# Performance work log

Measured on AMD Instinct MI355X. Metric: run time of the kernel, lower is better.

The kernel has to match this reference:

```python
import jax, jax.numpy as jnp
import numpy as np

TEMP = 0.07
EPS = 1e-6
NORM_EPS = 1e-12  # F.normalize default eps
LN_EPS = 1e-5

B, D, H, W = 32, 256, 64, 64
K = 256
DFF = 2048


def _l2norm(v, axis):
    n = jnp.sqrt(jnp.sum(v * v, axis=axis, keepdims=True))
    return v / jnp.maximum(n, NORM_EPS)


def _layernorm(v, g, b):
    mu = jnp.mean(v, axis=-1, keepdims=True)
    var = jnp.mean((v - mu) ** 2, axis=-1, keepdims=True)
    return (v - mu) * jax.lax.rsqrt(var + LN_EPS) * g + b


def setup_inputs() -> dict:
    key = jax.random.key(0)
    ks = jax.random.split(key, 8)
    s1 = 1.0 / np.sqrt(D)
    s2 = 1.0 / np.sqrt(DFF)
    return {
        "x": jax.random.normal(ks[0], (B, D, H, W), jnp.float32),
        "tgt": jax.random.normal(ks[1], (B, K, D), jnp.float32),
        "w1": jax.random.uniform(ks[2], (DFF, D), jnp.float32, -s1, s1),
        "b1": jax.random.uniform(ks[3], (DFF,), jnp.float32, -s1, s1),
        "w2": jax.random.uniform(ks[4], (D, DFF), jnp.float32, -s2, s2),
        "b2": jax.random.uniform(ks[5], (D,), jnp.float32, -s2, s2),
        "g2": jnp.ones((D,), jnp.float32),
        "be2": jnp.zeros((D,), jnp.float32),
        "g3": jnp.ones((D,), jnp.float32),
        "be3": jnp.zeros((D,), jnp.float32),
    }


def reference(x, tgt, w1, b1, w2, b2, g2, be2, g3, be3):
    # slot cross-attention with L2-normalized q/k
    tn = _l2norm(tgt, axis=2)           # (b,k,d)
    xn = _l2norm(x, axis=1)             # (b,d,h,w)
    dots = jnp.einsum('bkd,bdhw->bkhw', tn, xn)
    attn = jax.nn.softmax(dots / TEMP, axis=1) + EPS          # softmax over slots
    attn = attn / jnp.sum(attn, axis=(2, 3), keepdims=True)   # spatial normalization
    tgt2 = jnp.einsum('bdhw,bkhw->bkd', x, attn)
    t = _layernorm(tgt + tgt2, g2, be2)
    # FFN (dropout = identity in eval)
    ff = jnp.maximum(t @ w1.T + b1, 0.0) @ w2.T + b2
    return _layernorm(t + ff, g3, be3)
```

## Files before the change

kernel.cpp:

```cpp
#include <hip/hip_runtime.h>
#include <hip/hip_bf16.h>

using bf16 = __hip_bfloat16;

typedef __attribute__((ext_vector_type(8))) short short8;
typedef __attribute__((ext_vector_type(4))) float f32x4;

constexpr int Bb = 32, Dd = 256, HWw = 4096, Kk = 256, Ff = 2048;
constexpr float TEMP_INV = 1.0f / 0.07f;
constexpr float EPSf = 1e-6f;
constexpr float NORM_EPSf = 1e-12f;
constexpr float LN_EPSf = 1e-5f;

static __device__ __forceinline__ float b2f(bf16 v) { return __bfloat162float(v); }
static __device__ __forceinline__ bf16 f2b(float v) { return __float2bfloat16(v); }


__global__ __launch_bounds__(64) void k_tn(const float* __restrict__ tgt,
                                           bf16* __restrict__ tnbf) {
  int row = blockIdx.x;
  int b = row >> 8, slot = row & 255;
  int lane = threadIdx.x;
  const float* src = tgt + (size_t)row * Dd + lane * 4;
  float v[4];
#pragma unroll
  for (int u = 0; u < 4; u++) v[u] = src[u];
  float ss = v[0] * v[0] + v[1] * v[1] + v[2] * v[2] + v[3] * v[3];
#pragma unroll
  for (int m = 32; m >= 1; m >>= 1) ss += __shfl_xor(ss, m, 64);
  float inv = 1.0f / fmaxf(sqrtf(ss), NORM_EPSf);
  bf16 o[4] __attribute__((aligned(8)));
#pragma unroll
  for (int u = 0; u < 4; u++) o[u] = f2b(v[u] * inv);
  int s = lane >> 3;
  int q2 = (lane >> 1) & 3;
  int jh = (lane & 1) * 4;
  size_t fi = (size_t)((slot >> 4) * 64 + q2 * 16 + (slot & 15));
  *(float2*)(tnbf + ((size_t)(b * 8 + s) * 1024 + fi) * 8 + jh) = *(float2*)o;
}

__global__ __launch_bounds__(64) void k_prew1(const float* __restrict__ w1,
                                              bf16* __restrict__ w1bf) {
  int f = blockIdx.x;
  int lane = threadIdx.x;
  const float* src = w1 + (size_t)f * Dd + lane * 4;
  bf16 o[4] __attribute__((aligned(8)));
#pragma unroll
  for (int u = 0; u < 4; u++) o[u] = f2b(src[u]);
  int s = lane >> 3;
  int q2 = (lane >> 1) & 3;
  int jh = (lane & 1) * 4;
  size_t fi = (size_t)(((f & 63) >> 4) * 64 + q2 * 16 + (f & 15));
  *(float2*)(w1bf + ((size_t)((f >> 6) * 8 + s) * 256 + fi) * 8 + jh) = *(float2*)o;
}

__global__ __launch_bounds__(64) void k_prew2(const float* __restrict__ w2,
                                              bf16* __restrict__ w2bf) {
  int d = blockIdx.x;
  int lane = threadIdx.x;
  const float* src = w2 + (size_t)d * Ff + lane * 32;
  size_t gbase = (size_t)((d >> 6) * 64 + lane) * 256;
  int fbase = ((d & 63) >> 4) * 64 + (d & 15);
#pragma unroll
  for (int q2 = 0; q2 < 4; q2++) {
    float4 v0 = *(const float4*)(src + q2 * 8);
    float4 v1 = *(const float4*)(src + q2 * 8 + 4);
    bf16 o[8] __attribute__((aligned(16)));
    o[0] = f2b(v0.x); o[1] = f2b(v0.y); o[2] = f2b(v0.z); o[3] = f2b(v0.w);
    o[4] = f2b(v1.x); o[5] = f2b(v1.y); o[6] = f2b(v1.z); o[7] = f2b(v1.w);
    *(float4*)(w2bf + (gbase + fbase + q2 * 16) * 8) = *(float4*)o;
  }
}

#define MFMA16(a, b, c) __builtin_amdgcn_mfma_f32_16x16x32_bf16(a, b, c, 0, 0, 0)

__global__ __launch_bounds__(256) void k_dots(const bf16* __restrict__ tnbf,
                                              const float* __restrict__ x,
                                              bf16* __restrict__ xb_bf,
                                              bf16* __restrict__ attn_bf,
                                              float* __restrict__ S) {
  __shared__ __align__(16) char smem[23296];
  bf16* Bs = (bf16*)smem;
  float* ssred = (float*)(smem + 16640);
  float* nxl = (float*)(smem + 20992);
  float* red = (float*)(smem + 21248);
  int b = blockIdx.x >> 6;
  int hw0 = (blockIdx.x & 63) * 64;
  int tid = threadIdx.x;
  int wave = tid >> 6, lane = tid & 63;
  int quad = lane >> 4, nl = lane & 15;

  int dp = tid >> 4;
  int ch = tid & 15;
  int qb = dp >> 2;
  int jb = (dp & 3) * 2;

  f32x4 acc[4][4];
#pragma unroll
  for (int i = 0; i < 4; i++)
#pragma unroll
    for (int j = 0; j < 4; j++) acc[i][j] = (f32x4){0.f, 0.f, 0.f, 0.f};
  float ssp[4] = {0.f, 0.f, 0.f, 0.f};

  int spx = (hw0 >> 5) + (ch >> 3);
  int q2x = (ch >> 1) & 3;
  int jx = (ch & 1) * 4;

  float4 va4[2], vb4[2];
#pragma unroll
  for (int q = 0; q < 2; q++) {
    const float* xr = x + (size_t)((b << 8) + q * 32 + 2 * dp) * HWw + hw0 + ch * 4;
    va4[q] = *(const float4*)xr;
    vb4[q] = *(const float4*)(xr + HWw);
  }
  short8 afp[4];
  {
    const bf16* ts0 = tnbf + (size_t)(b * 8) * 1024 * 8;
#pragma unroll
    for (int mt = 0; mt < 4; mt++)
      afp[mt] = *(const short8*)(ts0 + (size_t)(((wave << 2) + mt) * 64 + lane) * 8);
  }

#pragma unroll 1
  for (int p = 0; p < 4; p++) {
    bf16* bsb = Bs + (p & 1) * 2 * 2080;
    bf16 paS[2][4] __attribute__((aligned(8)));
    bf16 pbS[2][4] __attribute__((aligned(8)));
#pragma unroll
    for (int q = 0; q < 2; q++) {
      float vva[4] = {va4[q].x, va4[q].y, va4[q].z, va4[q].w};
      float vvb[4] = {vb4[q].x, vb4[q].y, vb4[q].z, vb4[q].w};
#pragma unroll
      for (int jj = 0; jj < 4; jj++) {
        ssp[jj] += vva[jj] * vva[jj] + vvb[jj] * vvb[jj];
        paS[q][jj] = f2b(vva[jj]);
        pbS[q][jj] = f2b(vvb[jj]);
      }
#pragma unroll
      for (int jj = 0; jj < 4; jj++) {
        int hwl = ch * 4 + jj;
        int nt = hwl >> 4;
        int li = (qb << 4) | (hwl & 15);
        union { bf16 h[2]; unsigned int u; } pk;
        pk.h[0] = paS[q][jj];
        pk.h[1] = pbS[q][jj];
        *(unsigned int*)&bsb[q * 2080 + nt * 520 + li * 8 + jb] = pk.u;
      }
    }
    __syncthreads();

    if (p < 3) {
#pragma unroll
      for (int q = 0; q < 2; q++) {
        const float* xr = x + (size_t)((b << 8) + ((p + 1) * 2 + q) * 32 + 2 * dp) * HWw + hw0 + ch * 4;
        va4[q] = *(const float4*)xr;
        vb4[q] = *(const float4*)(xr + HWw);
      }
    }
#pragma unroll
    for (int q = 0; q < 2; q++) {
      int s = 2 * p + q;
      int d0r = s * 32 + 2 * dp;
      int fiA = (d0r >> 4) * 64 + q2x * 16 + (d0r & 15);
      size_t base = ((size_t)(b * 128) + spx) * 1024;
      *(float2*)(xb_bf + (base + fiA) * 8 + jx) = *(float2*)paS[q];
      *(float2*)(xb_bf + (base + fiA + 1) * 8 + jx) = *(float2*)pbS[q];
    }
#pragma unroll
    for (int q = 0; q < 2; q++) {
      int s = 2 * p + q;
      short8 af[4];
#pragma unroll
      for (int mt = 0; mt < 4; mt++) af[mt] = afp[mt];
      if (s < 7) {
        const bf16* tsrc = tnbf + (size_t)(b * 8 + s + 1) * 1024 * 8;
#pragma unroll
        for (int mt = 0; mt < 4; mt++)
          afp[mt] = *(const short8*)(tsrc + (size_t)(((wave << 2) + mt) * 64 + lane) * 8);
      }
      short8 bfv[4];
#pragma unroll
      for (int nt = 0; nt < 4; nt++)
        bfv[nt] = *(const short8*)(bsb + q * 2080 + nt * 520 + lane * 8);
#pragma unroll
      for (int mt = 0; mt < 4; mt++)
#pragma unroll
        for (int nt = 0; nt < 4; nt++) acc[mt][nt] = MFMA16(af[mt], bfv[nt], acc[mt][nt]);
    }
  }

#pragma unroll
  for (int jj = 0; jj < 4; jj++) ssred[(ch * 4 + jj) * 17 + dp] = ssp[jj];
  __syncthreads();
  if (tid < 64) {
    float sum = 0.f;
#pragma unroll
    for (int i = 0; i < 16; i++) sum += ssred[tid * 17 + i];
    nxl[tid] = TEMP_INV / fmaxf(sqrtf(sum), NORM_EPSf);
  }
  __syncthreads();

  float sc[4];
#pragma unroll
  for (int nt = 0; nt < 4; nt++) sc[nt] = nxl[nt * 16 + nl];
#pragma unroll
  for (int mt = 0; mt < 4; mt++)
#pragma unroll
    for (int nt = 0; nt < 4; nt++)
#pragma unroll
      for (int r = 0; r < 4; r++) acc[mt][nt][r] *= sc[nt];

  float* red2 = red + 256;

  float pmax[4];
#pragma unroll
  for (int nt = 0; nt < 4; nt++) {
    float m = acc[0][nt][0];
#pragma unroll
    for (int mt = 0; mt < 4; mt++)
#pragma unroll
      for (int r = 0; r < 4; r++) m = fmaxf(m, acc[mt][nt][r]);
    m = fmaxf(m, __shfl_xor(m, 16, 64));
    m = fmaxf(m, __shfl_xor(m, 32, 64));
    pmax[nt] = m;
  }
  if (lane < 16) {
#pragma unroll
    for (int nt = 0; nt < 4; nt++) red[((wave << 2) + nt) * 16 + nl] = pmax[nt];
  }
  __syncthreads();
  float cmax[4];
#pragma unroll
  for (int nt = 0; nt < 4; nt++) {
    float m = red[nt * 16 + nl];
#pragma unroll
    for (int w2 = 1; w2 < 4; w2++) m = fmaxf(m, red[((w2 << 2) + nt) * 16 + nl]);
    cmax[nt] = m;
  }

  float psum[4];
#pragma unroll
  for (int nt = 0; nt < 4; nt++) {
    float s = 0.f;
#pragma unroll
    for (int mt = 0; mt < 4; mt++)
#pragma unroll
      for (int r = 0; r < 4; r++) {
        float e = __expf(acc[mt][nt][r] - cmax[nt]);
        acc[mt][nt][r] = e;
        s += e;
      }
    s += __shfl_xor(s, 16, 64);
    s += __shfl_xor(s, 32, 64);
    psum[nt] = s;
  }
  if (lane < 16) {
#pragma unroll
    for (int nt = 0; nt < 4; nt++) red2[((wave << 2) + nt) * 16 + nl] = psum[nt];
  }
  __syncthreads();
  float ci[4];
#pragma unroll
  for (int nt = 0; nt < 4; nt++) {
    float s = 0.f;
#pragma unroll
    for (int w2 = 0; w2 < 4; w2++) s += red2[((w2 << 2) + nt) * 16 + nl];
    ci[nt] = 1.0f / s;
  }

#pragma unroll
  for (int mt = 0; mt < 4; mt++) {
    int slotg = (b << 8) + (wave << 6) + (mt << 4) + (quad << 2);
#pragma unroll
    for (int r = 0; r < 4; r++) {
      float rs = 0.f;
#pragma unroll
      for (int nt = 0; nt < 4; nt++) {
        bf16 hb = f2b(acc[mt][nt][r] * ci[nt] + EPSf);
        float q = b2f(hb);
        acc[mt][nt][r] = q;
        rs += q;
      }
      rs += __shfl_xor(rs, 1, 64);
      rs += __shfl_xor(rs, 2, 64);
      rs += __shfl_xor(rs, 4, 64);
      rs += __shfl_xor(rs, 8, 64);
      if (nl == 0) atomicAdd(&S[slotg + r], rs);
    }
  }

  __syncthreads();
  bf16* rp = (bf16*)smem;
  int jat = nl & 7;
#pragma unroll
  for (int h = 0; h < 2; h++) {
#pragma unroll
    for (int mt = 0; mt < 4; mt++) {
      int fi0 = ((wave << 2) + mt) * 64 + (quad << 2);
#pragma unroll
      for (int ntl = 0; ntl < 2; ntl++) {
        int nt = (h << 1) + ntl;
        int q2p = (ntl << 1) + (nl >> 3);
#pragma unroll
        for (int r = 0; r < 4; r++) {
          int fi = fi0 + q2p * 16 + r;
          int fisw = fi ^ ((fi >> 3) & 3);
          rp[fisw * 8 + jat] = f2b(acc[mt][nt][r]);
        }
      }
    }
    __syncthreads();
    size_t gbase = ((size_t)(b * 128) + (hw0 >> 5) + h) * 1024 * 8;
#pragma unroll
    for (int u = 0; u < 4; u++) {
      int fl = u * 256 + tid;
      int fg = fl ^ ((fl >> 3) & 3);
      short8 vv = *(const short8*)(rp + (size_t)fl * 8);
      *(short8*)(attn_bf + gbase + (size_t)fg * 8) = vv;
    }
    if (h == 0) __syncthreads();
  }
}

__global__ __launch_bounds__(256) void k_gemm2(const bf16* __restrict__ attn_bf,
                                               const bf16* __restrict__ xb_bf,
                                               float* __restrict__ t2) {
  int n = blockIdx.x;
  int b = n & 31;
  int r2 = n >> 5;
  int kp = r2 & 3;
  int dgrp = r2 >> 2;
  int tid = threadIdx.x;
  int wave = tid >> 6, lane = tid & 63;
  int wr = wave >> 1, wc = wave & 1;

  f32x4 acc[2][2];
#pragma unroll
  for (int i = 0; i < 2; i++)
#pragma unroll
    for (int j = 0; j < 2; j++) acc[i][j] = (f32x4){0.f, 0.f, 0.f, 0.f};

  const bf16* Abase = attn_bf + ((size_t)(b * 128) * 1024 + (size_t)(kp * 4 + wr * 2) * 64) * 8;
  const bf16* Bbase = xb_bf + ((size_t)(b * 128) * 1024 + (size_t)(dgrp * 4 + wc * 2) * 64) * 8;
#pragma unroll 4
  for (int st = 0; st < 128; st++) {
    const bf16* Ap = Abase + (size_t)st * 1024 * 8;
    const bf16* Bp = Bbase + (size_t)st * 1024 * 8;
    short8 a0 = *(const short8*)(Ap + (size_t)lane * 8);
    short8 a1 = *(const short8*)(Ap + (size_t)(64 + lane) * 8);
    short8 b0 = *(const short8*)(Bp + (size_t)lane * 8);
    short8 b1 = *(const short8*)(Bp + (size_t)(64 + lane) * 8);
    acc[0][0] = MFMA16(a0, b0, acc[0][0]);
    acc[0][1] = MFMA16(a0, b1, acc[0][1]);
    acc[1][0] = MFMA16(a1, b0, acc[1][0]);
    acc[1][1] = MFMA16(a1, b1, acc[1][1]);
  }
  int quad = lane >> 4, nl = lane & 15;
#pragma unroll
  for (int i = 0; i < 2; i++)
#pragma unroll
    for (int r = 0; r < 4; r++) {
      int row = (b << 8) + kp * 64 + wr * 32 + i * 16 + quad * 4 + r;
#pragma unroll
      for (int j = 0; j < 2; j++) {
        int col = dgrp * 64 + wc * 32 + j * 16 + nl;
        t2[(size_t)row * Dd + col] = acc[i][j][r];
      }
    }
}

__global__ __launch_bounds__(64) void k_ln_pre(const float* __restrict__ t2,
                                               const float* __restrict__ S,
                                               const float* __restrict__ tgt,
                                               const float* __restrict__ g,
                                               const float* __restrict__ be,
                                               float* __restrict__ t,
                                               bf16* __restrict__ tbf) {
  int row = blockIdx.x;
  int lane = threadIdx.x;
  float sInv = 1.0f / S[row];
  size_t off = (size_t)row * Dd + lane * 4;
  float4 a0 = *(const float4*)(t2 + off);
  const float* pt = tgt + off;
  float v[4];
  v[0] = a0.x * sInv + pt[0];
  v[1] = a0.y * sInv + pt[1];
  v[2] = a0.z * sInv + pt[2];
  v[3] = a0.w * sInv + pt[3];
  float s1 = v[0] + v[1] + v[2] + v[3];
  float s2 = v[0] * v[0] + v[1] * v[1] + v[2] * v[2] + v[3] * v[3];
#pragma unroll
  for (int m = 32; m >= 1; m >>= 1) {
    s1 += __shfl_xor(s1, m, 64);
    s2 += __shfl_xor(s2, m, 64);
  }
  float mu = s1 * (1.0f / 256.0f);
  float var = s2 * (1.0f / 256.0f) - mu * mu;
  float rs = rsqrtf(fmaxf(var, 0.f) + LN_EPSf);
  float* po = t + (size_t)row * Dd + lane * 4;
  bf16 o[4] __attribute__((aligned(8)));
#pragma unroll
  for (int u = 0; u < 4; u++) {
    float val = (v[u] - mu) * rs * g[lane * 4 + u] + be[lane * 4 + u];
    po[u] = val;
    o[u] = f2b(val);
  }
  int s = lane >> 3;
  int q2 = (lane >> 1) & 3;
  int jh = (lane & 1) * 4;
  size_t fi = (size_t)(((row & 63) >> 4) * 64 + q2 * 16 + (row & 15));
  *(float2*)(tbf + ((size_t)((row >> 6) * 8 + s) * 256 + fi) * 8 + jh) = *(float2*)o;
}

__global__ __launch_bounds__(256) void k_ffn1(const bf16* __restrict__ tbf,
                                              const bf16* __restrict__ w1bf,
                                              const float* __restrict__ b1,
                                              bf16* __restrict__ h1bf) {
  __shared__ __align__(16) bf16 rp[512 * 8];
  int rowgrp = blockIdx.x >> 5;
  int fgrp = blockIdx.x & 31;
  int tid = threadIdx.x;
  int wave = tid >> 6, lane = tid & 63;
  int am = (wave >> 1) * 2, bn = (wave & 1) * 2;

  f32x4 acc[2][2];
#pragma unroll
  for (int i = 0; i < 2; i++)
#pragma unroll
    for (int j = 0; j < 2; j++) acc[i][j] = (f32x4){0.f, 0.f, 0.f, 0.f};

  const bf16* Abase = tbf + (size_t)rowgrp * 8 * 256 * 8;
  const bf16* Bbase = w1bf + (size_t)fgrp * 8 * 256 * 8;
#pragma unroll
  for (int s = 0; s < 8; s++) {
    short8 af[2], bfr[2];
#pragma unroll
    for (int i = 0; i < 2; i++)
      af[i] = *(const short8*)(Abase + ((size_t)s * 256 + ((am + i) * 64 + lane)) * 8);
#pragma unroll
    for (int j = 0; j < 2; j++)
      bfr[j] = *(const short8*)(Bbase + ((size_t)s * 256 + ((bn + j) * 64 + lane)) * 8);
#pragma unroll
    for (int i = 0; i < 2; i++)
#pragma unroll
      for (int j = 0; j < 2; j++) acc[i][j] = MFMA16(af[i], bfr[j], acc[i][j]);
  }
  int quad = lane >> 4, nl = lane & 15;
  int jat = nl & 7;
#pragma unroll
  for (int j = 0; j < 2; j++) {
    int f = fgrp * 64 + (bn + j) * 16 + nl;
    float bias = b1[f];
    int seth = (bn + j) >> 1;
    int q2p = ((bn + j) & 1) * 2 + (nl >> 3);
#pragma unroll
    for (int i = 0; i < 2; i++) {
      int fiBase = (am + i) * 64 + q2p * 16 + (quad << 2);
#pragma unroll
      for (int r = 0; r < 4; r++) {
        float val = fmaxf(acc[i][j][r] + bias, 0.f);
        int fi = fiBase + r;
        int fisw = fi ^ ((fi >> 3) & 3);
        rp[(seth * 256 + fisw) * 8 + jat] = f2b(val);
      }
    }
  }
  __syncthreads();
  size_t sp0 = (size_t)(rowgrp * 64) + fgrp * 2;
#pragma unroll
  for (int u = 0; u < 2; u++) {
    int loc = tid;
    int fg = loc ^ ((loc >> 3) & 3);
    short8 vv = *(const short8*)(rp + ((size_t)u * 256 + loc) * 8);
    *(short8*)(h1bf + ((sp0 + u) * 256 + fg) * 8) = vv;
  }
}

__global__ __launch_bounds__(256) void k_ffn2(const bf16* __restrict__ h1bf,
                                              const bf16* __restrict__ w2bf,
                                              float* __restrict__ o2) {
  __shared__ float redsm[4 * 4160];
  int n = blockIdx.x;
  int rowgrp = n >> 2;
  int cg = n & 3;
  int tid = threadIdx.x;
  int wave = tid >> 6, lane = tid & 63;

  f32x4 acc[4][4];
#pragma unroll
  for (int i = 0; i < 4; i++)
#pragma unroll
    for (int j = 0; j < 4; j++) acc[i][j] = (f32x4){0.f, 0.f, 0.f, 0.f};

#pragma unroll 4
  for (int stl = 0; stl < 16; stl++) {
    int sg = wave * 16 + stl;
    const bf16* Ab = h1bf + ((size_t)(rowgrp * 64 + sg) * 256) * 8;
    const bf16* Bbv = w2bf + ((size_t)(cg * 64 + sg) * 256) * 8;
    short8 af[4], bfr[4];
#pragma unroll
    for (int mt = 0; mt < 4; mt++)
      af[mt] = *(const short8*)(Ab + (size_t)(mt * 64 + lane) * 8);
#pragma unroll
    for (int nt = 0; nt < 4; nt++)
      bfr[nt] = *(const short8*)(Bbv + (size_t)(nt * 64 + lane) * 8);
#pragma unroll
    for (int mt = 0; mt < 4; mt++)
#pragma unroll
      for (int nt = 0; nt < 4; nt++) acc[mt][nt] = MFMA16(af[mt], bfr[nt], acc[mt][nt]);
  }
  int quad = lane >> 4, nl = lane & 15;
  float* my = redsm + wave * 4160;
#pragma unroll
  for (int mt = 0; mt < 4; mt++)
#pragma unroll
    for (int r = 0; r < 4; r++) {
      int row = mt * 16 + quad * 4 + r;
#pragma unroll
      for (int nt = 0; nt < 4; nt++)
        my[row * 65 + nt * 16 + nl] = acc[mt][nt][r];
    }
  __syncthreads();
#pragma unroll
  for (int u = 0; u < 16; u++) {
    int o = u * 256 + tid;
    int row = o >> 6, col = o & 63;
    int li = row * 65 + col;
    float ssum = redsm[li] + redsm[4160 + li] + redsm[8320 + li] + redsm[12480 + li];
    o2[(size_t)(rowgrp * 64 + row) * Dd + cg * 64 + col] = ssum;
  }
}

__global__ __launch_bounds__(64) void k_ln_out(const float* __restrict__ o2,
                                               const float* __restrict__ b2v,
                                               const float* __restrict__ t,
                                               const float* __restrict__ g,
                                               const float* __restrict__ be,
                                               float* __restrict__ out) {
  int row = blockIdx.x;
  int lane = threadIdx.x;
  size_t off = (size_t)row * Dd + lane * 4;
  float4 aq = *(const float4*)(o2 + off);
  const float* pt = t + off;
  float v[4];
  v[0] = aq.x + b2v[lane * 4 + 0] + pt[0];
  v[1] = aq.y + b2v[lane * 4 + 1] + pt[1];
  v[2] = aq.z + b2v[lane * 4 + 2] + pt[2];
  v[3] = aq.w + b2v[lane * 4 + 3] + pt[3];
  float s1 = v[0] + v[1] + v[2] + v[3];
  float s2 = v[0] * v[0] + v[1] * v[1] + v[2] * v[2] + v[3] * v[3];
#pragma unroll
  for (int m = 32; m >= 1; m >>= 1) {
    s1 += __shfl_xor(s1, m, 64);
    s2 += __shfl_xor(s2, m, 64);
  }
  float mu = s1 * (1.0f / 256.0f);
  float var = s2 * (1.0f / 256.0f) - mu * mu;
  float rs = rsqrtf(fmaxf(var, 0.f) + LN_EPSf);
  float* pw = out + (size_t)row * Dd + lane * 4;
#pragma unroll
  for (int u = 0; u < 4; u++)
    pw[u] = (v[u] - mu) * rs * g[lane * 4 + u] + be[lane * 4 + u];
}

extern "C" void kernel_launch(void* const* d_in, const int* in_sizes, int n_in,
                              void* d_out, int out_size, void* d_ws, size_t ws_size,
                              hipStream_t stream) {
  const float* x = (const float*)d_in[0];
  const float* tgt = (const float*)d_in[1];
  const float* w1 = (const float*)d_in[2];
  const float* b1 = (const float*)d_in[3];
  const float* w2 = (const float*)d_in[4];
  const float* b2v = (const float*)d_in[5];
  const float* g2 = (const float*)d_in[6];
  const float* be2 = (const float*)d_in[7];
  const float* g3 = (const float*)d_in[8];
  const float* be3 = (const float*)d_in[9];
  float* out = (float*)d_out;

  char* w = (char*)d_ws;
  bf16* tnbf = (bf16*)w;     w += (size_t)Bb * Kk * Dd * 2;
  float* S = (float*)w;      w += (size_t)Bb * Kk * 4;
  float* t = (float*)w;      w += (size_t)Bb * Kk * Dd * 4;
  bf16* attn_bf = (bf16*)w;  w += (size_t)Bb * HWw * Kk * 2;
  bf16* h1bf = (bf16*)w;     w += (size_t)Bb * Kk * Ff * 2;
  bf16* xb_bf = (bf16*)w;    w += (size_t)Bb * Dd * HWw * 2;

  bf16* tbf = tnbf;
  bf16* w1bf = attn_bf;
  bf16* w2bf = attn_bf + (size_t)Ff * Dd;
  float* t2 = (float*)h1bf;
  float* o2 = (float*)xb_bf;

  hipMemsetAsync(S, 0, (size_t)Bb * Kk * 4, stream);
  k_tn<<<Bb * Kk, 64, 0, stream>>>(tgt, tnbf);
  k_dots<<<Bb * (HWw / 64), 256, 0, stream>>>(tnbf, x, xb_bf, attn_bf, S);
  k_gemm2<<<512, 256, 0, stream>>>(attn_bf, xb_bf, t2);
  k_prew1<<<Ff, 64, 0, stream>>>(w1, w1bf);
  k_prew2<<<Dd, 64, 0, stream>>>(w2, w2bf);
  k_ln_pre<<<Bb * Kk, 64, 0, stream>>>(t2, S, tgt, g2, be2, t, tbf);
  k_ffn1<<<(Bb * Kk / 64) * (Ff / 64), 256, 0, stream>>>(tbf, w1bf, b1, h1bf);
  k_ffn2<<<512, 256, 0, stream>>>(h1bf, w2bf, o2);
  k_ln_out<<<Bb * Kk, 64, 0, stream>>>(o2, b2v, t, g3, be3, out);
}
```

Baseline: 391.1 us.

## Split gemm2 into smaller per-block tiles and tune k_dots occupancy and prefetch

k_gemm2 now gives each wave a 16x32 output tile instead of 32x32, which doubles the grid to 1024 blocks (dgrp now spans 8 groups of 32 columns). The goal is more parallelism and fewer stalls in the latency-bound reduction over the 4096-long spatial axis, at the cost of reloading each B tile more often. k_dots gets a launch-bounds hint asking for 3 blocks per SM, a hoisted x base pointer, and the next-x prefetch moved after the xb_bf stores. That lowers register pressure, but the prefetch now has less time to overlap with other work.

```diff
diff --git a/kernel.cpp b/kernel.cpp
--- a/kernel.cpp
+++ b/kernel.cpp
@@ -74,11 +74,11 @@
 
 #define MFMA16(a, b, c) __builtin_amdgcn_mfma_f32_16x16x32_bf16(a, b, c, 0, 0, 0)
 
-__global__ __launch_bounds__(256) void k_dots(const bf16* __restrict__ tnbf,
-                                              const float* __restrict__ x,
-                                              bf16* __restrict__ xb_bf,
-                                              bf16* __restrict__ attn_bf,
-                                              float* __restrict__ S) {
+__global__ __launch_bounds__(256, 3) void k_dots(const bf16* __restrict__ tnbf,
+                                                 const float* __restrict__ x,
+                                                 bf16* __restrict__ xb_bf,
+                                                 bf16* __restrict__ attn_bf,
+                                                 float* __restrict__ S) {
   __shared__ __align__(16) char smem[23296];
   bf16* Bs = (bf16*)smem;
   float* ssred = (float*)(smem + 16640);
@@ -106,10 +106,11 @@
   int q2x = (ch >> 1) & 3;
   int jx = (ch & 1) * 4;
 
+  const float* xbase = x + (size_t)((b << 8) + 2 * dp) * HWw + hw0 + ch * 4;
   float4 va4[2], vb4[2];
 #pragma unroll
   for (int q = 0; q < 2; q++) {
-    const float* xr = x + (size_t)((b << 8) + q * 32 + 2 * dp) * HWw + hw0 + ch * 4;
+    const float* xr = xbase + (size_t)(q * 32) * HWw;
     va4[q] = *(const float4*)xr;
     vb4[q] = *(const float4*)(xr + HWw);
   }
@@ -149,14 +150,6 @@
     }
     __syncthreads();
 
-    if (p < 3) {
-#pragma unroll
-      for (int q = 0; q < 2; q++) {
-        const float* xr = x + (size_t)((b << 8) + ((p + 1) * 2 + q) * 32 + 2 * dp) * HWw + hw0 + ch * 4;
-        va4[q] = *(const float4*)xr;
-        vb4[q] = *(const float4*)(xr + HWw);
-      }
-    }
 #pragma unroll
     for (int q = 0; q < 2; q++) {
       int s = 2 * p + q;
@@ -165,6 +158,14 @@
       size_t base = ((size_t)(b * 128) + spx) * 1024;
       *(float2*)(xb_bf + (base + fiA) * 8 + jx) = *(float2*)paS[q];
       *(float2*)(xb_bf + (base + fiA + 1) * 8 + jx) = *(float2*)pbS[q];
+    }
+    if (p < 3) {
+#pragma unroll
+      for (int q = 0; q < 2; q++) {
+        const float* xr = xbase + (size_t)(((p + 1) * 2 + q) * 32) * HWw;
+        va4[q] = *(const float4*)xr;
+        vb4[q] = *(const float4*)(xr + HWw);
+      }
     }
 #pragma unroll
     for (int q = 0; q < 2; q++) {
@@ -332,41 +333,33 @@
   int dgrp = r2 >> 2;
   int tid = threadIdx.x;
   int wave = tid >> 6, lane = tid & 63;
-  int wr = wave >> 1, wc = wave & 1;
-
-  f32x4 acc[2][2];
-#pragma unroll
-  for (int i = 0; i < 2; i++)
-#pragma unroll
-    for (int j = 0; j < 2; j++) acc[i][j] = (f32x4){0.f, 0.f, 0.f, 0.f};
-
-  const bf16* Abase = attn_bf + ((size_t)(b * 128) * 1024 + (size_t)(kp * 4 + wr * 2) * 64) * 8;
-  const bf16* Bbase = xb_bf + ((size_t)(b * 128) * 1024 + (size_t)(dgrp * 4 + wc * 2) * 64) * 8;
+
+  f32x4 acc[2];
+  acc[0] = (f32x4){0.f, 0.f, 0.f, 0.f};
+  acc[1] = (f32x4){0.f, 0.f, 0.f, 0.f};
+
+  const bf16* Abase = attn_bf + ((size_t)(b * 128) * 1024 + (size_t)(kp * 4 + wave) * 64) * 8;
+  const bf16* Bbase = xb_bf + ((size_t)(b * 128) * 1024 + (size_t)(dgrp * 2) * 64) * 8;
 #pragma unroll 4
   for (int st = 0; st < 128; st++) {
     const bf16* Ap = Abase + (size_t)st * 1024 * 8;
     const bf16* Bp = Bbase + (size_t)st * 1024 * 8;
     short8 a0 = *(const short8*)(Ap + (size_t)lane * 8);
-    short8 a1 = *(const short8*)(Ap + (size_t)(64 + lane) * 8);
     short8 b0 = *(const short8*)(Bp + (size_t)lane * 8);
     short8 b1 = *(const short8*)(Bp + (size_t)(64 + lane) * 8);
-    acc[0][0] = MFMA16(a0, b0, acc[0][0]);
-    acc[0][1] = MFMA16(a0, b1, acc[0][1]);
-    acc[1][0] = MFMA16(a1, b0, acc[1][0]);
-    acc[1][1] = MFMA16(a1, b1, acc[1][1]);
+    acc[0] = MFMA16(a0, b0, acc[0]);
+    acc[1] = MFMA16(a0, b1, acc[1]);
   }
   int quad = lane >> 4, nl = lane & 15;
 #pragma unroll
-  for (int i = 0; i < 2; i++)
-#pragma unroll
-    for (int r = 0; r < 4; r++) {
-      int row = (b << 8) + kp * 64 + wr * 32 + i * 16 + quad * 4 + r;
-#pragma unroll
-      for (int j = 0; j < 2; j++) {
-        int col = dgrp * 64 + wc * 32 + j * 16 + nl;
-        t2[(size_t)row * Dd + col] = acc[i][j][r];
-      }
-    }
+  for (int r = 0; r < 4; r++) {
+    int row = (b << 8) + kp * 64 + wave * 16 + quad * 4 + r;
+#pragma unroll
+    for (int j = 0; j < 2; j++) {
+      int col = dgrp * 32 + j * 16 + nl;
+      t2[(size_t)row * Dd + col] = acc[j][r];
+    }
+  }
 }
 
 __global__ __launch_bounds__(64) void k_ln_pre(const float* __restrict__ t2,
@@ -595,7 +588,7 @@
   hipMemsetAsync(S, 0, (size_t)Bb * Kk * 4, stream);
   k_tn<<<Bb * Kk, 64, 0, stream>>>(tgt, tnbf);
   k_dots<<<Bb * (HWw / 64), 256, 0, stream>>>(tnbf, x, xb_bf, attn_bf, S);
-  k_gemm2<<<512, 256, 0, stream>>>(attn_bf, xb_bf, t2);
+  k_gemm2<<<1024, 256, 0, stream>>>(attn_bf, xb_bf, t2);
   k_prew1<<<Ff, 64, 0, stream>>>(w1, w1bf);
   k_prew2<<<Dd, 64, 0, stream>>>(w2, w2bf);
   k_ln_pre<<<Bb * Kk, 64, 0, stream>>>(t2, S, tgt, g2, be2, t, tbf);
```

New measurement: 397.0 us. No clear change (+1.5%).
